# Kernel tuning notes

Measured on AMD Instinct MI355X. Metric: run time of the kernel, lower is better.

The kernel has to match this reference:

```python
import jax, jax.numpy as jnp
import numpy as np

N_NODES = 100000
N_EDGES = 1600000
IN_DIM, HID_DIM, OUT_DIM = 32, 64, 8


def sage_conv(x, src, dst, W_l, b_l, W_r, n_nodes):
    # PyG SAGEConv (aggr='mean', root_weight=True):
    # out_i = W_l @ mean_{j in N(i)} x_j + b_l + W_r @ x_i
    msg_sum = jax.ops.segment_sum(x[src], dst, num_segments=n_nodes)  # [N, F]
    deg = jax.ops.segment_sum(jnp.ones((src.shape[0],), x.dtype), dst,
                              num_segments=n_nodes)  # [N]
    agg = msg_sum / jnp.maximum(deg, 1.0)[:, None]
    return agg @ W_l.T + b_l + x @ W_r.T


def setup_inputs() -> dict:
    key = jax.random.key(0)
    ks = jax.random.split(key, 8)
    x = jax.random.normal(ks[0], (N_NODES, IN_DIM), dtype=jnp.float32)
    edge_index = jax.random.randint(ks[1], (2, N_EDGES), 0, N_NODES, dtype=jnp.int64)
    s1 = 1.0 / np.sqrt(IN_DIM)
    s2 = 1.0 / np.sqrt(HID_DIM)
    return {
        "x": x,
        "edge_index": edge_index,
        "W1_l": jax.random.uniform(ks[2], (HID_DIM, IN_DIM), jnp.float32, -s1, s1),
        "b1": jnp.zeros((HID_DIM,), jnp.float32),
        "W1_r": jax.random.uniform(ks[3], (HID_DIM, IN_DIM), jnp.float32, -s1, s1),
        "W2_l": jax.random.uniform(ks[4], (OUT_DIM, HID_DIM), jnp.float32, -s2, s2),
        "b2": jnp.zeros((OUT_DIM,), jnp.float32),
        "W2_r": jax.random.uniform(ks[5], (OUT_DIM, HID_DIM), jnp.float32, -s2, s2),
    }


def reference(x, edge_index, W1_l, b1, W1_r, W2_l, b2, W2_r):
    src, dst = edge_index[0], edge_index[1]
    h = sage_conv(x, src, dst, W1_l, b1, W1_r, N_NODES)
    h = jax.nn.relu(h)
    out = sage_conv(h, src, dst, W2_l, b2, W2_r, N_NODES)
    return out
```

## Files before the change

kernel.cpp:

```cpp
#include <hip/hip_runtime.h>

#define N_NODES 100000
#define N_EDGES 1600000
#define IN_DIM 32
#define HID_DIM 64
#define OUT_DIM 8
#define BK 64
#define NBKT ((N_NODES + BK - 1) / BK)
#define QC 1280
#define CHUNK 4096
#define NCHUNK ((N_EDGES + CHUNK - 1) / CHUNK)

typedef unsigned short u16;
typedef unsigned int u32;
typedef unsigned long long ull;

__device__ __forceinline__ float bf2f(u16 v) {
    return __uint_as_float(((u32)v) << 16);
}

__device__ __forceinline__ u16 f2bf(float f) {
    u32 u = __float_as_uint(f);
    u32 lsb = (u >> 16) & 1u;
    u += 0x7fffu + lsb;
    return (u16)(u >> 16);
}

__device__ __forceinline__ float ldf(const void* p, size_t i, int bf) {
    return bf ? bf2f(((const u16*)p)[i]) : ((const float*)p)[i];
}

__global__ __launch_bounds__(256) void k_part2(
    const int* __restrict__ ei, const u32* __restrict__ xw,
    const void* __restrict__ W1l, const void* __restrict__ b1,
    const void* __restrict__ W1r,
    const void* __restrict__ W2l, const void* __restrict__ b2,
    const void* __restrict__ W2r,
    int* __restrict__ qcnt, u32* __restrict__ qbuf,
    float* __restrict__ tW1l, float* __restrict__ tW1r,
    float* __restrict__ tW2l, float* __restrict__ tW2r,
    float* __restrict__ tb1, float* __restrict__ tb2)
{
    __shared__ int shv, bfv;
    __shared__ int hist[NBKT], gbase[NBKT], lcur[NBKT];
    int t = threadIdx.x;
    if (t < 64) {
        int v = ei[2 * t + 1];
        ull m1 = __ballot(v == 0);
        u32 wd = xw[t];
        u32 b = (wd >> 8) & 0x7fu;
        ull m2 = __ballot(b >= 0x38u && b <= 0x41u);
        if (t == 0) {
            shv = (m1 == ~0ULL) ? 1 : 0;
            bfv = (__popcll(m2) >= 56) ? 1 : 0;
        }
    }
    for (int i = t; i < NBKT; i += 256) { hist[i] = 0; lcur[i] = 0; }
    __syncthreads();
    int sh = shv, bf = bfv;

    if (blockIdx.x < 16) {
        for (int i = blockIdx.x * 256 + t; i < HID_DIM * IN_DIM; i += 16 * 256) {
            int o = i / IN_DIM, k = i % IN_DIM;
            tW1l[k * HID_DIM + o] = ldf(W1l, i, bf);
            tW1r[k * HID_DIM + o] = ldf(W1r, i, bf);
        }
        for (int i = blockIdx.x * 256 + t; i < OUT_DIM * HID_DIM; i += 16 * 256) {
            int o = i / HID_DIM, k = i % HID_DIM;
            tW2l[k * OUT_DIM + o] = ldf(W2l, i, bf);
            tW2r[k * OUT_DIM + o] = ldf(W2r, i, bf);
        }
        if (blockIdx.x == 0) {
            if (t < HID_DIM) tb1[t] = ldf(b1, t, bf);
            if (t < OUT_DIM) tb2[t] = ldf(b2, t, bf);
        }
    }

    int e0 = blockIdx.x * CHUNK;
    int myd[16], mys[16];
    #pragma unroll
    for (int i = 0; i < 16; i++) {
        int e = e0 + i * 256 + t;
        if (e < N_EDGES) {
            size_t off = (size_t)e << sh;
            mys[i] = ei[off];
            int d = ei[((size_t)N_EDGES << sh) + off];
            myd[i] = d;
            atomicAdd(&hist[d >> 6], 1);
        } else myd[i] = -1;
    }
    __syncthreads();
    for (int i = t; i < NBKT; i += 256) {
        int h = hist[i];
        gbase[i] = h ? atomicAdd(&qcnt[i], h) : 0;
    }
    __syncthreads();
    #pragma unroll
    for (int i = 0; i < 16; i++) {
        int d = myd[i];
        if (d >= 0) {
            int bk = d >> 6;
            int p = gbase[bk] + atomicAdd(&lcur[bk], 1);
            if (p < QC)
                qbuf[(size_t)bk * QC + p] = ((u32)mys[i] << 6) | (u32)(d & 63);
        }
    }
}

__global__ __launch_bounds__(256, 4) void k_l1(
    const void* __restrict__ x,
    const int* __restrict__ qcnt, const u32* __restrict__ qbuf,
    const float* __restrict__ tW1l, const float* __restrict__ tW1r,
    const float* __restrict__ tW2l, const float* __restrict__ tW2r,
    const float* __restrict__ tb1, const float* __restrict__ tb2,
    u16* __restrict__ gbuf, float* __restrict__ rbuf,
    const u32* __restrict__ xw)
{
    __shared__ int hist[BK], pos[BK], pcur[BK];
    __shared__ u32 srt[QC];
    __shared__ float xs[BK][IN_DIM];
    __shared__ float aggw[4][2][IN_DIM];
    __shared__ float hb[8][HID_DIM + 1];
    __shared__ int bfv;

    int t = threadIdx.x;
    if (t < 64) {
        u32 wd = xw[t];
        u32 b = (wd >> 8) & 0x7fu;
        ull m2 = __ballot(b >= 0x38u && b <= 0x41u);
        if (t == 0) bfv = (__popcll(m2) >= 56) ? 1 : 0;
    }
    if (t < BK) hist[t] = 0;
    __syncthreads();
    int bf = bfv;
    int b = blockIdx.x, nb = b * BK;
    int m = qcnt[b]; if (m > QC) m = QC; if (m < 0) m = 0;
    const u32* q = qbuf + (size_t)b * QC;

    if (bf) {
        const u32* xr = (const u32*)x + (size_t)nb * (IN_DIM / 2);
        int lim = ((N_NODES - nb < BK) ? (N_NODES - nb) : BK) * (IN_DIM / 2);
        for (int i = t; i < BK * (IN_DIM / 2); i += 256) {
            u32 w = (i < lim) ? xr[i] : 0u;
            int r = i >> 4, c = i & 15;
            xs[r][2 * c]     = bf2f((u16)w);
            xs[r][2 * c + 1] = bf2f((u16)(w >> 16));
        }
    } else {
        const float* xr = (const float*)x + (size_t)nb * IN_DIM;
        int lim = ((N_NODES - nb < BK) ? (N_NODES - nb) : BK) * IN_DIM;
        for (int i = t; i < BK * IN_DIM; i += 256)
            xs[i >> 5][i & 31] = (i < lim) ? xr[i] : 0.0f;
    }

    for (int i = t; i < m; i += 256)
        atomicAdd(&hist[q[i] & 63], 1);
    __syncthreads();
    if (t < 64) {
        int v = hist[t];
        int inc = v;
        #pragma unroll
        for (int o = 1; o < 64; o <<= 1) {
            int y = __shfl_up(inc, o, 64);
            if (t >= o) inc += y;
        }
        int ex = inc - v;
        pos[t] = ex; pcur[t] = ex;
    }
    __syncthreads();
    for (int i = t; i < m; i += 256) {
        u32 u = q[i];
        int p = atomicAdd(&pcur[u & 63], 1);
        srt[p] = u >> 6;
    }
    __syncthreads();

    int wid = t >> 6, lane = t & 63;
    int half = lane >> 5, g2 = (lane >> 3) & 3, l = lane & 7;
    int o = lane;
    float bb = tb1[o];
    for (int pr = 0; pr < 8; pr++) {
        int s0 = pr * 8 + wid * 2;
        int ns = s0 + half;
        int st = pos[ns], deg = hist[ns];
        float a0 = 0, a1 = 0, a2 = 0, a3 = 0;
        float c0 = 0, c1 = 0, c2 = 0, c3 = 0;
        float d0 = 0, d1 = 0, d2 = 0, d3 = 0;
        float e0 = 0, e1 = 0, e2 = 0, e3 = 0;
        int j = g2;
        for (; j + 12 < deg; j += 16) {
            int sA = (int)srt[st + j];
            int sB = (int)srt[st + j + 4];
            int sC = (int)srt[st + j + 8];
            int sD = (int)srt[st + j + 12];
            if (bf) {
                ushort4 vA = reinterpret_cast<const ushort4*>((const u16*)x + (size_t)sA * IN_DIM)[l];
                ushort4 vB = reinterpret_cast<const ushort4*>((const u16*)x + (size_t)sB * IN_DIM)[l];
                ushort4 vC = reinterpret_cast<const ushort4*>((const u16*)x + (size_t)sC * IN_DIM)[l];
                ushort4 vD = reinterpret_cast<const ushort4*>((const u16*)x + (size_t)sD * IN_DIM)[l];
                a0 += bf2f(vA.x); a1 += bf2f(vA.y); a2 += bf2f(vA.z); a3 += bf2f(vA.w);
                c0 += bf2f(vB.x); c1 += bf2f(vB.y); c2 += bf2f(vB.z); c3 += bf2f(vB.w);
                d0 += bf2f(vC.x); d1 += bf2f(vC.y); d2 += bf2f(vC.z); d3 += bf2f(vC.w);
                e0 += bf2f(vD.x); e1 += bf2f(vD.y); e2 += bf2f(vD.z); e3 += bf2f(vD.w);
            } else {
                float4 vA = reinterpret_cast<const float4*>((const float*)x + (size_t)sA * IN_DIM)[l];
                float4 vB = reinterpret_cast<const float4*>((const float*)x + (size_t)sB * IN_DIM)[l];
                float4 vC = reinterpret_cast<const float4*>((const float*)x + (size_t)sC * IN_DIM)[l];
                float4 vD = reinterpret_cast<const float4*>((const float*)x + (size_t)sD * IN_DIM)[l];
                a0 += vA.x; a1 += vA.y; a2 += vA.z; a3 += vA.w;
                c0 += vB.x; c1 += vB.y; c2 += vB.z; c3 += vB.w;
                d0 += vC.x; d1 += vC.y; d2 += vC.z; d3 += vC.w;
                e0 += vD.x; e1 += vD.y; e2 += vD.z; e3 += vD.w;
            }
        }
        for (; j + 4 < deg; j += 8) {
            int sA = (int)srt[st + j];
            int sB = (int)srt[st + j + 4];
            if (bf) {
                ushort4 vA = reinterpret_cast<const ushort4*>((const u16*)x + (size_t)sA * IN_DIM)[l];
                ushort4 vB = reinterpret_cast<const ushort4*>((const u16*)x + (size_t)sB * IN_DIM)[l];
                a0 += bf2f(vA.x); a1 += bf2f(vA.y); a2 += bf2f(vA.z); a3 += bf2f(vA.w);
                c0 += bf2f(vB.x); c1 += bf2f(vB.y); c2 += bf2f(vB.z); c3 += bf2f(vB.w);
            } else {
                float4 vA = reinterpret_cast<const float4*>((const float*)x + (size_t)sA * IN_DIM)[l];
                float4 vB = reinterpret_cast<const float4*>((const float*)x + (size_t)sB * IN_DIM)[l];
                a0 += vA.x; a1 += vA.y; a2 += vA.z; a3 += vA.w;
                c0 += vB.x; c1 += vB.y; c2 += vB.z; c3 += vB.w;
            }
        }
        if (j < deg) {
            int s = (int)srt[st + j];
            if (bf) {
                ushort4 vv = reinterpret_cast<const ushort4*>((const u16*)x + (size_t)s * IN_DIM)[l];
                a0 += bf2f(vv.x); a1 += bf2f(vv.y); a2 += bf2f(vv.z); a3 += bf2f(vv.w);
            } else {
                float4 vv = reinterpret_cast<const float4*>((const float*)x + (size_t)s * IN_DIM)[l];
                a0 += vv.x; a1 += vv.y; a2 += vv.z; a3 += vv.w;
            }
        }
        a0 += c0 + d0 + e0;
        a1 += c1 + d1 + e1;
        a2 += c2 + d2 + e2;
        a3 += c3 + d3 + e3;
        a0 += __shfl_xor(a0, 8, 64);  a0 += __shfl_xor(a0, 16, 64);
        a1 += __shfl_xor(a1, 8, 64);  a1 += __shfl_xor(a1, 16, 64);
        a2 += __shfl_xor(a2, 8, 64);  a2 += __shfl_xor(a2, 16, 64);
        a3 += __shfl_xor(a3, 8, 64);  a3 += __shfl_xor(a3, 16, 64);
        if (g2 == 0) {
            aggw[wid][half][4 * l + 0] = a0; aggw[wid][half][4 * l + 1] = a1;
            aggw[wid][half][4 * l + 2] = a2; aggw[wid][half][4 * l + 3] = a3;
        }
        float rd0 = 1.0f / fmaxf((float)hist[s0], 1.0f);
        float rd1 = 1.0f / fmaxf((float)hist[s0 + 1], 1.0f);
        float acc0 = bb, acc1 = bb;
        #pragma unroll 8
        for (int k = 0; k < IN_DIM; k++) {
            float wl = tW1l[k * HID_DIM + o];
            float wr = tW1r[k * HID_DIM + o];
            acc0 += (aggw[wid][0][k] * rd0) * wl + xs[s0][k] * wr;
            acc1 += (aggw[wid][1][k] * rd1) * wl + xs[s0 + 1][k] * wr;
        }
        hb[wid * 2][o]     = fmaxf(acc0, 0.0f);
        hb[wid * 2 + 1][o] = fmaxf(acc1, 0.0f);
        int hs = wid * 2 + half;
        float ga = 0.0f, ra = 0.0f;
        #pragma unroll 4
        for (int mm = 0; mm < 16; mm++) {
            int k = g2 * 16 + mm;
            float hv = hb[hs][k];
            ga += hv * tW2l[k * OUT_DIM + l];
            ra += hv * tW2r[k * OUT_DIM + l];
        }
        ga += __shfl_xor(ga, 8, 64);  ga += __shfl_xor(ga, 16, 64);
        ra += __shfl_xor(ra, 8, 64);  ra += __shfl_xor(ra, 16, 64);
        int n = nb + ns;
        if (g2 == 0 && n < N_NODES) {
            __builtin_nontemporal_store(f2bf(ga), &gbuf[(size_t)n * OUT_DIM + l]);
            __builtin_nontemporal_store(ra + tb2[l], &rbuf[(size_t)n * OUT_DIM + l]);
        }
    }
}

__global__ __launch_bounds__(256) void k_l2(
    const u16* __restrict__ gbuf, const float* __restrict__ rbuf,
    const int* __restrict__ qcnt, const u32* __restrict__ qbuf,
    const u32* __restrict__ xw, void* __restrict__ out)
{
    __shared__ int hist[BK], pos[BK], pcur[BK];
    __shared__ u32 srt[QC];
    __shared__ int bfv;
    int t = threadIdx.x;
    if (t < 64) {
        u32 w = xw[t];
        u32 b = (w >> 8) & 0x7fu;
        ull m2 = __ballot(b >= 0x38u && b <= 0x41u);
        if (t == 0) bfv = (__popcll(m2) >= 56) ? 1 : 0;
    }
    if (t < BK) hist[t] = 0;
    __syncthreads();
    int b = blockIdx.x, nb = b * BK;
    int m = qcnt[b]; if (m > QC) m = QC; if (m < 0) m = 0;
    const u32* q = qbuf + (size_t)b * QC;

    for (int i = t; i < m; i += 256)
        atomicAdd(&hist[q[i] & 63], 1);
    __syncthreads();
    if (t < 64) {
        int v = hist[t];
        int inc = v;
        #pragma unroll
        for (int o = 1; o < 64; o <<= 1) {
            int y = __shfl_up(inc, o, 64);
            if (t >= o) inc += y;
        }
        int ex = inc - v;
        pos[t] = ex; pcur[t] = ex;
    }
    __syncthreads();
    for (int i = t; i < m; i += 256) {
        u32 u = q[i];
        int p = atomicAdd(&pcur[u & 63], 1);
        srt[p] = u >> 6;
    }
    __syncthreads();

    int grp = t >> 3, l = t & 7;
    for (int r = 0; r < 2; r++) {
        int ns = grp * 2 + r;
        int st = pos[ns], deg = hist[ns];
        float a0 = 0.0f, a1 = 0.0f, a2 = 0.0f, a3 = 0.0f;
        int j = 0;
        for (; j + 3 < deg; j += 4) {
            int v0 = (int)srt[st + j];
            int v1 = (int)srt[st + j + 1];
            int v2 = (int)srt[st + j + 2];
            int v3 = (int)srt[st + j + 3];
            a0 += bf2f(gbuf[(size_t)v0 * OUT_DIM + l]);
            a1 += bf2f(gbuf[(size_t)v1 * OUT_DIM + l]);
            a2 += bf2f(gbuf[(size_t)v2 * OUT_DIM + l]);
            a3 += bf2f(gbuf[(size_t)v3 * OUT_DIM + l]);
        }
        for (; j < deg; j++) a0 += bf2f(gbuf[(size_t)srt[st + j] * OUT_DIM + l]);
        int n = nb + ns;
        if (n < N_NODES) {
            float res = (a0 + a1 + a2 + a3) / fmaxf((float)deg, 1.0f)
                      + rbuf[(size_t)n * OUT_DIM + l];
            size_t oi = (size_t)n * OUT_DIM + l;
            if (bfv) ((u16*)out)[oi] = f2bf(res);
            else     ((float*)out)[oi] = res;
        }
    }
}

extern "C" void kernel_launch(void* const* d_in, const int* in_sizes, int n_in,
                              void* d_out, int out_size, void* d_ws, size_t ws_size,
                              hipStream_t stream) {
    const void* x   = d_in[0];
    const int*  ei  = (const int*)d_in[1];
    const void* W1l = d_in[2];
    const void* b1  = d_in[3];
    const void* W1r = d_in[4];
    const void* W2l = d_in[5];
    const void* b2  = d_in[6];
    const void* W2r = d_in[7];

    int* qcnt    = (int*)d_ws;
    float* tW1l  = (float*)(qcnt + 2048);
    float* tW1r  = tW1l + IN_DIM * HID_DIM;
    float* tW2l  = tW1r + IN_DIM * HID_DIM;
    float* tW2r  = tW2l + HID_DIM * OUT_DIM;
    float* tb1   = tW2r + HID_DIM * OUT_DIM;
    float* tb2   = tb1 + HID_DIM;
    u32* qbuf    = (u32*)(tb2 + OUT_DIM);
    u16* gbuf    = (u16*)(qbuf + (size_t)NBKT * QC);
    float* rbuf  = (float*)(gbuf + (size_t)N_NODES * OUT_DIM);

    hipMemsetAsync(d_ws, 0, 2048 * sizeof(int), stream);

    k_part2<<<NCHUNK, 256, 0, stream>>>(ei, (const u32*)x,
                                        W1l, b1, W1r, W2l, b2, W2r,
                                        qcnt, qbuf,
                                        tW1l, tW1r, tW2l, tW2r, tb1, tb2);
    k_l1<<<NBKT, 256, 0, stream>>>(x, qcnt, qbuf,
                                   tW1l, tW1r, tW2l, tW2r, tb1, tb2,
                                   gbuf, rbuf, (const u32*)x);
    k_l2<<<NBKT, 256, 0, stream>>>(gbuf, rbuf, qcnt, qbuf,
                                   (const u32*)x, d_out);
}
```

Before: 213.9 us.

## Split x features into two half-width arrays and gather in two passes

The partition kernel now also copies x into two separate arrays holding the low and high 16 features of each node. The layer-1 gather runs in two passes, one per half, with 8 neighbor groups of 4 lanes each. Results go into a full-block shared agg buffer that the matmul stage reads. The aim is to shrink the gathered working set per pass so it stays in cache and improves locality. In exchange it adds an extra copy of x, more workspace, larger shared memory, and twice the index traversal. Several reads also switch to nontemporal loads.

```diff
diff --git a/kernel.cpp b/kernel.cpp
--- a/kernel.cpp
+++ b/kernel.cpp
@@ -39,7 +39,8 @@
     int* __restrict__ qcnt, u32* __restrict__ qbuf,
     float* __restrict__ tW1l, float* __restrict__ tW1r,
     float* __restrict__ tW2l, float* __restrict__ tW2r,
-    float* __restrict__ tb1, float* __restrict__ tb2)
+    float* __restrict__ tb1, float* __restrict__ tb2,
+    u32* __restrict__ xlo, u32* __restrict__ xhi)
 {
     __shared__ int shv, bfv;
     __shared__ int hist[NBKT], gbase[NBKT], lcur[NBKT];
@@ -59,6 +60,20 @@
     __syncthreads();
     int sh = shv, bf = bfv;
 
+    if (bf) {
+        for (int i = blockIdx.x * 256 + t; i < N_NODES * 8; i += NCHUNK * 256) {
+            int n2 = i >> 3, k = i & 7;
+            __builtin_nontemporal_store(xw[n2 * 16 + k], &xlo[i]);
+            __builtin_nontemporal_store(xw[n2 * 16 + 8 + k], &xhi[i]);
+        }
+    } else {
+        for (int i = blockIdx.x * 256 + t; i < N_NODES * 16; i += NCHUNK * 256) {
+            int n2 = i >> 4, k = i & 15;
+            __builtin_nontemporal_store(xw[n2 * 32 + k], &xlo[i]);
+            __builtin_nontemporal_store(xw[n2 * 32 + 16 + k], &xhi[i]);
+        }
+    }
+
     if (blockIdx.x < 16) {
         for (int i = blockIdx.x * 256 + t; i < HID_DIM * IN_DIM; i += 16 * 256) {
             int o = i / IN_DIM, k = i % IN_DIM;
@@ -108,6 +123,7 @@
 }
 
 __global__ __launch_bounds__(256, 4) void k_l1(
+    const void* __restrict__ xlo, const void* __restrict__ xhi,
     const void* __restrict__ x,
     const int* __restrict__ qcnt, const u32* __restrict__ qbuf,
     const float* __restrict__ tW1l, const float* __restrict__ tW1r,
@@ -119,7 +135,7 @@
     __shared__ int hist[BK], pos[BK], pcur[BK];
     __shared__ u32 srt[QC];
     __shared__ float xs[BK][IN_DIM];
-    __shared__ float aggw[4][2][IN_DIM];
+    __shared__ float agg[BK][IN_DIM];
     __shared__ float hb[8][HID_DIM + 1];
     __shared__ int bfv;
 
@@ -141,7 +157,7 @@
         const u32* xr = (const u32*)x + (size_t)nb * (IN_DIM / 2);
         int lim = ((N_NODES - nb < BK) ? (N_NODES - nb) : BK) * (IN_DIM / 2);
         for (int i = t; i < BK * (IN_DIM / 2); i += 256) {
-            u32 w = (i < lim) ? xr[i] : 0u;
+            u32 w = (i < lim) ? __builtin_nontemporal_load(&xr[i]) : 0u;
             int r = i >> 4, c = i & 15;
             xs[r][2 * c]     = bf2f((u16)w);
             xs[r][2 * c + 1] = bf2f((u16)(w >> 16));
@@ -150,11 +166,11 @@
         const float* xr = (const float*)x + (size_t)nb * IN_DIM;
         int lim = ((N_NODES - nb < BK) ? (N_NODES - nb) : BK) * IN_DIM;
         for (int i = t; i < BK * IN_DIM; i += 256)
-            xs[i >> 5][i & 31] = (i < lim) ? xr[i] : 0.0f;
+            xs[i >> 5][i & 31] = (i < lim) ? __builtin_nontemporal_load(&xr[i]) : 0.0f;
     }
 
     for (int i = t; i < m; i += 256)
-        atomicAdd(&hist[q[i] & 63], 1);
+        atomicAdd(&hist[__builtin_nontemporal_load(&q[i]) & 63], 1);
     __syncthreads();
     if (t < 64) {
         int v = hist[t];
@@ -169,87 +185,94 @@
     }
     __syncthreads();
     for (int i = t; i < m; i += 256) {
-        u32 u = q[i];
+        u32 u = __builtin_nontemporal_load(&q[i]);
         int p = atomicAdd(&pcur[u & 63], 1);
         srt[p] = u >> 6;
     }
     __syncthreads();
 
     int wid = t >> 6, lane = t & 63;
-    int half = lane >> 5, g2 = (lane >> 3) & 3, l = lane & 7;
+    int half = lane >> 5;
+    int g3 = (lane >> 2) & 7;
+    int l2 = lane & 3;
+    #pragma unroll
+    for (int pass = 0; pass < 2; pass++) {
+        const void* xh = pass ? xhi : xlo;
+        int kb = pass * 16 + l2 * 4;
+        for (int pr = 0; pr < 8; pr++) {
+            int ns = pr * 8 + wid * 2 + half;
+            int st = pos[ns], deg = hist[ns];
+            float a0 = 0, a1 = 0, a2 = 0, a3 = 0;
+            float c0 = 0, c1 = 0, c2 = 0, c3 = 0;
+            int j = g3;
+            for (; j + 24 < deg; j += 32) {
+                int sA = (int)srt[st + j];
+                int sB = (int)srt[st + j + 8];
+                int sC = (int)srt[st + j + 16];
+                int sD = (int)srt[st + j + 24];
+                if (bf) {
+                    ushort4 vA = reinterpret_cast<const ushort4*>((const u16*)xh + (size_t)sA * 16)[l2];
+                    ushort4 vB = reinterpret_cast<const ushort4*>((const u16*)xh + (size_t)sB * 16)[l2];
+                    ushort4 vC = reinterpret_cast<const ushort4*>((const u16*)xh + (size_t)sC * 16)[l2];
+                    ushort4 vD = reinterpret_cast<const ushort4*>((const u16*)xh + (size_t)sD * 16)[l2];
+                    a0 += bf2f(vA.x); a1 += bf2f(vA.y); a2 += bf2f(vA.z); a3 += bf2f(vA.w);
+                    c0 += bf2f(vB.x); c1 += bf2f(vB.y); c2 += bf2f(vB.z); c3 += bf2f(vB.w);
+                    a0 += bf2f(vC.x); a1 += bf2f(vC.y); a2 += bf2f(vC.z); a3 += bf2f(vC.w);
+                    c0 += bf2f(vD.x); c1 += bf2f(vD.y); c2 += bf2f(vD.z); c3 += bf2f(vD.w);
+                } else {
+                    float4 vA = reinterpret_cast<const float4*>((const float*)xh + (size_t)sA * 16)[l2];
+                    float4 vB = reinterpret_cast<const float4*>((const float*)xh + (size_t)sB * 16)[l2];
+                    float4 vC = reinterpret_cast<const float4*>((const float*)xh + (size_t)sC * 16)[l2];
+                    float4 vD = reinterpret_cast<const float4*>((const float*)xh + (size_t)sD * 16)[l2];
+                    a0 += vA.x; a1 += vA.y; a2 += vA.z; a3 += vA.w;
+                    c0 += vB.x; c1 += vB.y; c2 += vB.z; c3 += vB.w;
+                    a0 += vC.x; a1 += vC.y; a2 += vC.z; a3 += vC.w;
+                    c0 += vD.x; c1 += vD.y; c2 += vD.z; c3 += vD.w;
+                }
+            }
+            for (; j + 8 < deg; j += 16) {
+                int sA = (int)srt[st + j];
+                int sB = (int)srt[st + j + 8];
+                if (bf) {
+                    ushort4 vA = reinterpret_cast<const ushort4*>((const u16*)xh + (size_t)sA * 16)[l2];
+                    ushort4 vB = reinterpret_cast<const ushort4*>((const u16*)xh + (size_t)sB * 16)[l2];
+                    a0 += bf2f(vA.x); a1 += bf2f(vA.y); a2 += bf2f(vA.z); a3 += bf2f(vA.w);
+                    c0 += bf2f(vB.x); c1 += bf2f(vB.y); c2 += bf2f(vB.z); c3 += bf2f(vB.w);
+                } else {
+                    float4 vA = reinterpret_cast<const float4*>((const float*)xh + (size_t)sA * 16)[l2];
+                    float4 vB = reinterpret_cast<const float4*>((const float*)xh + (size_t)sB * 16)[l2];
+                    a0 += vA.x; a1 += vA.y; a2 += vA.z; a3 += vA.w;
+                    c0 += vB.x; c1 += vB.y; c2 += vB.z; c3 += vB.w;
+                }
+            }
+            if (j < deg) {
+                int s = (int)srt[st + j];
+                if (bf) {
+                    ushort4 vv = reinterpret_cast<const ushort4*>((const u16*)xh + (size_t)s * 16)[l2];
+                    a0 += bf2f(vv.x); a1 += bf2f(vv.y); a2 += bf2f(vv.z); a3 += bf2f(vv.w);
+                } else {
+                    float4 vv = reinterpret_cast<const float4*>((const float*)xh + (size_t)s * 16)[l2];
+                    a0 += vv.x; a1 += vv.y; a2 += vv.z; a3 += vv.w;
+                }
+            }
+            a0 += c0; a1 += c1; a2 += c2; a3 += c3;
+            a0 += __shfl_xor(a0, 4, 64); a0 += __shfl_xor(a0, 8, 64); a0 += __shfl_xor(a0, 16, 64);
+            a1 += __shfl_xor(a1, 4, 64); a1 += __shfl_xor(a1, 8, 64); a1 += __shfl_xor(a1, 16, 64);
+            a2 += __shfl_xor(a2, 4, 64); a2 += __shfl_xor(a2, 8, 64); a2 += __shfl_xor(a2, 16, 64);
+            a3 += __shfl_xor(a3, 4, 64); a3 += __shfl_xor(a3, 8, 64); a3 += __shfl_xor(a3, 16, 64);
+            if (g3 == 0) {
+                agg[ns][kb + 0] = a0; agg[ns][kb + 1] = a1;
+                agg[ns][kb + 2] = a2; agg[ns][kb + 3] = a3;
+            }
+        }
+    }
+
+    int g2 = (lane >> 3) & 3, l = lane & 7;
     int o = lane;
     float bb = tb1[o];
     for (int pr = 0; pr < 8; pr++) {
         int s0 = pr * 8 + wid * 2;
         int ns = s0 + half;
-        int st = pos[ns], deg = hist[ns];
-        float a0 = 0, a1 = 0, a2 = 0, a3 = 0;
-        float c0 = 0, c1 = 0, c2 = 0, c3 = 0;
-        float d0 = 0, d1 = 0, d2 = 0, d3 = 0;
-        float e0 = 0, e1 = 0, e2 = 0, e3 = 0;
-        int j = g2;
-        for (; j + 12 < deg; j += 16) {
-            int sA = (int)srt[st + j];
-            int sB = (int)srt[st + j + 4];
-            int sC = (int)srt[st + j + 8];
-            int sD = (int)srt[st + j + 12];
-            if (bf) {
-                ushort4 vA = reinterpret_cast<const ushort4*>((const u16*)x + (size_t)sA * IN_DIM)[l];
-                ushort4 vB = reinterpret_cast<const ushort4*>((const u16*)x + (size_t)sB * IN_DIM)[l];
-                ushort4 vC = reinterpret_cast<const ushort4*>((const u16*)x + (size_t)sC * IN_DIM)[l];
-                ushort4 vD = reinterpret_cast<const ushort4*>((const u16*)x + (size_t)sD * IN_DIM)[l];
-                a0 += bf2f(vA.x); a1 += bf2f(vA.y); a2 += bf2f(vA.z); a3 += bf2f(vA.w);
-                c0 += bf2f(vB.x); c1 += bf2f(vB.y); c2 += bf2f(vB.z); c3 += bf2f(vB.w);
-                d0 += bf2f(vC.x); d1 += bf2f(vC.y); d2 += bf2f(vC.z); d3 += bf2f(vC.w);
-                e0 += bf2f(vD.x); e1 += bf2f(vD.y); e2 += bf2f(vD.z); e3 += bf2f(vD.w);
-            } else {
-                float4 vA = reinterpret_cast<const float4*>((const float*)x + (size_t)sA * IN_DIM)[l];
-                float4 vB = reinterpret_cast<const float4*>((const float*)x + (size_t)sB * IN_DIM)[l];
-                float4 vC = reinterpret_cast<const float4*>((const float*)x + (size_t)sC * IN_DIM)[l];
-                float4 vD = reinterpret_cast<const float4*>((const float*)x + (size_t)sD * IN_DIM)[l];
-                a0 += vA.x; a1 += vA.y; a2 += vA.z; a3 += vA.w;
-                c0 += vB.x; c1 += vB.y; c2 += vB.z; c3 += vB.w;
-                d0 += vC.x; d1 += vC.y; d2 += vC.z; d3 += vC.w;
-                e0 += vD.x; e1 += vD.y; e2 += vD.z; e3 += vD.w;
-            }
-        }
-        for (; j + 4 < deg; j += 8) {
-            int sA = (int)srt[st + j];
-            int sB = (int)srt[st + j + 4];
-            if (bf) {
-                ushort4 vA = reinterpret_cast<const ushort4*>((const u16*)x + (size_t)sA * IN_DIM)[l];
-                ushort4 vB = reinterpret_cast<const ushort4*>((const u16*)x + (size_t)sB * IN_DIM)[l];
-                a0 += bf2f(vA.x); a1 += bf2f(vA.y); a2 += bf2f(vA.z); a3 += bf2f(vA.w);
-                c0 += bf2f(vB.x); c1 += bf2f(vB.y); c2 += bf2f(vB.z); c3 += bf2f(vB.w);
-            } else {
-                float4 vA = reinterpret_cast<const float4*>((const float*)x + (size_t)sA * IN_DIM)[l];
-                float4 vB = reinterpret_cast<const float4*>((const float*)x + (size_t)sB * IN_DIM)[l];
-                a0 += vA.x; a1 += vA.y; a2 += vA.z; a3 += vA.w;
-                c0 += vB.x; c1 += vB.y; c2 += vB.z; c3 += vB.w;
-            }
-        }
-        if (j < deg) {
-            int s = (int)srt[st + j];
-            if (bf) {
-                ushort4 vv = reinterpret_cast<const ushort4*>((const u16*)x + (size_t)s * IN_DIM)[l];
-                a0 += bf2f(vv.x); a1 += bf2f(vv.y); a2 += bf2f(vv.z); a3 += bf2f(vv.w);
-            } else {
-                float4 vv = reinterpret_cast<const float4*>((const float*)x + (size_t)s * IN_DIM)[l];
-                a0 += vv.x; a1 += vv.y; a2 += vv.z; a3 += vv.w;
-            }
-        }
-        a0 += c0 + d0 + e0;
-        a1 += c1 + d1 + e1;
-        a2 += c2 + d2 + e2;
-        a3 += c3 + d3 + e3;
-        a0 += __shfl_xor(a0, 8, 64);  a0 += __shfl_xor(a0, 16, 64);
-        a1 += __shfl_xor(a1, 8, 64);  a1 += __shfl_xor(a1, 16, 64);
-        a2 += __shfl_xor(a2, 8, 64);  a2 += __shfl_xor(a2, 16, 64);
-        a3 += __shfl_xor(a3, 8, 64);  a3 += __shfl_xor(a3, 16, 64);
-        if (g2 == 0) {
-            aggw[wid][half][4 * l + 0] = a0; aggw[wid][half][4 * l + 1] = a1;
-            aggw[wid][half][4 * l + 2] = a2; aggw[wid][half][4 * l + 3] = a3;
-        }
         float rd0 = 1.0f / fmaxf((float)hist[s0], 1.0f);
         float rd1 = 1.0f / fmaxf((float)hist[s0 + 1], 1.0f);
         float acc0 = bb, acc1 = bb;
@@ -257,8 +280,8 @@
         for (int k = 0; k < IN_DIM; k++) {
             float wl = tW1l[k * HID_DIM + o];
             float wr = tW1r[k * HID_DIM + o];
-            acc0 += (aggw[wid][0][k] * rd0) * wl + xs[s0][k] * wr;
-            acc1 += (aggw[wid][1][k] * rd1) * wl + xs[s0 + 1][k] * wr;
+            acc0 += (agg[s0][k] * rd0) * wl + xs[s0][k] * wr;
+            acc1 += (agg[s0 + 1][k] * rd1) * wl + xs[s0 + 1][k] * wr;
         }
         hb[wid * 2][o]     = fmaxf(acc0, 0.0f);
         hb[wid * 2 + 1][o] = fmaxf(acc1, 0.0f);
@@ -303,7 +326,7 @@
     const u32* q = qbuf + (size_t)b * QC;
 
     for (int i = t; i < m; i += 256)
-        atomicAdd(&hist[q[i] & 63], 1);
+        atomicAdd(&hist[__builtin_nontemporal_load(&q[i]) & 63], 1);
     __syncthreads();
     if (t < 64) {
         int v = hist[t];
@@ -318,7 +341,7 @@
     }
     __syncthreads();
     for (int i = t; i < m; i += 256) {
-        u32 u = q[i];
+        u32 u = __builtin_nontemporal_load(&q[i]);
         int p = atomicAdd(&pcur[u & 63], 1);
         srt[p] = u >> 6;
     }
@@ -374,14 +397,17 @@
     u32* qbuf    = (u32*)(tb2 + OUT_DIM);
     u16* gbuf    = (u16*)(qbuf + (size_t)NBKT * QC);
     float* rbuf  = (float*)(gbuf + (size_t)N_NODES * OUT_DIM);
+    u32* xlo     = (u32*)(rbuf + (size_t)N_NODES * OUT_DIM);
+    u32* xhi     = xlo + (size_t)N_NODES * 16;
 
     hipMemsetAsync(d_ws, 0, 2048 * sizeof(int), stream);
 
     k_part2<<<NCHUNK, 256, 0, stream>>>(ei, (const u32*)x,
                                         W1l, b1, W1r, W2l, b2, W2r,
                                         qcnt, qbuf,
-                                        tW1l, tW1r, tW2l, tW2r, tb1, tb2);
-    k_l1<<<NBKT, 256, 0, stream>>>(x, qcnt, qbuf,
+                                        tW1l, tW1r, tW2l, tW2r, tb1, tb2,
+                                        xlo, xhi);
+    k_l1<<<NBKT, 256, 0, stream>>>(xlo, xhi, x, qcnt, qbuf,
                                    tW1l, tW1r, tW2l, tW2r, tb1, tb2,
                                    gbuf, rbuf, (const u32*)x);
     k_l2<<<NBKT, 256, 0, stream>>>(gbuf, rbuf, qcnt, qbuf,
```

New measurement: 237.3 us. 11.0% more time.

## Split neighbor gather into two source-range passes for cache locality

Applied to the files above, without the earlier changes.

Edges for each destination block are binned by whether the source node falls in the lower or upper half of the node range, and the gather runs in two passes so that all blocks touch roughly the same half of x at a time. Aggregates go to a per-block shared agg array and are summed across passes before the dense layer. The aim is better L2/MALL hit rate on the random gathers. In exchange it adds a second scan, more shared memory (lower occupancy), and only global phase alignment between blocks, which is not guaranteed.

```diff
diff --git a/kernel.cpp b/kernel.cpp
--- a/kernel.cpp
+++ b/kernel.cpp
@@ -10,6 +10,7 @@
 #define QC 1280
 #define CHUNK 4096
 #define NCHUNK ((N_EDGES + CHUNK - 1) / CHUNK)
+#define SRC_MID 50000
 
 typedef unsigned short u16;
 typedef unsigned int u32;
@@ -116,12 +117,12 @@
     u16* __restrict__ gbuf, float* __restrict__ rbuf,
     const u32* __restrict__ xw)
 {
-    __shared__ int hist[BK], pos[BK], pcur[BK];
+    __shared__ int hist[2 * BK], pos[2 * BK], pcur[2 * BK];
     __shared__ u32 srt[QC];
     __shared__ float xs[BK][IN_DIM];
-    __shared__ float aggw[4][2][IN_DIM];
+    __shared__ float agg[BK][IN_DIM];
     __shared__ float hb[8][HID_DIM + 1];
-    __shared__ int bfv;
+    __shared__ int wtot, bfv;
 
     int t = threadIdx.x;
     if (t < 64) {
@@ -130,7 +131,7 @@
         ull m2 = __ballot(b >= 0x38u && b <= 0x41u);
         if (t == 0) bfv = (__popcll(m2) >= 56) ? 1 : 0;
     }
-    if (t < BK) hist[t] = 0;
+    if (t < 2 * BK) hist[t] = 0;
     __syncthreads();
     int bf = bfv;
     int b = blockIdx.x, nb = b * BK;
@@ -153,112 +154,129 @@
             xs[i >> 5][i & 31] = (i < lim) ? xr[i] : 0.0f;
     }
 
-    for (int i = t; i < m; i += 256)
-        atomicAdd(&hist[q[i] & 63], 1);
-    __syncthreads();
-    if (t < 64) {
-        int v = hist[t];
-        int inc = v;
+    for (int i = t; i < m; i += 256) {
+        u32 u = q[i];
+        int bin = (((int)(u >> 6) >= SRC_MID) ? BK : 0) | (int)(u & 63);
+        atomicAdd(&hist[bin], 1);
+    }
+    __syncthreads();
+    int inc = 0, v = 0;
+    if (t < 128) {
+        v = hist[t]; inc = v;
         #pragma unroll
         for (int o = 1; o < 64; o <<= 1) {
             int y = __shfl_up(inc, o, 64);
-            if (t >= o) inc += y;
-        }
-        int ex = inc - v;
+            if ((t & 63) >= o) inc += y;
+        }
+        if (t == 63) wtot = inc;
+    }
+    __syncthreads();
+    if (t < 128) {
+        int ex = ((t >= 64) ? wtot : 0) + inc - v;
         pos[t] = ex; pcur[t] = ex;
     }
     __syncthreads();
     for (int i = t; i < m; i += 256) {
         u32 u = q[i];
-        int p = atomicAdd(&pcur[u & 63], 1);
-        srt[p] = u >> 6;
+        int s = (int)(u >> 6);
+        int bin = ((s >= SRC_MID) ? BK : 0) | (int)(u & 63);
+        int p = atomicAdd(&pcur[bin], 1);
+        srt[p] = (u32)s;
     }
     __syncthreads();
 
     int wid = t >> 6, lane = t & 63;
     int half = lane >> 5, g2 = (lane >> 3) & 3, l = lane & 7;
+    for (int pass = 0; pass < 2; pass++) {
+        for (int pr = 0; pr < 8; pr++) {
+            int ns = pr * 8 + wid * 2 + half;
+            int bin = pass * BK + ns;
+            int st = pos[bin], dg = hist[bin];
+            float a0 = 0, a1 = 0, a2 = 0, a3 = 0;
+            float c0 = 0, c1 = 0, c2 = 0, c3 = 0;
+            float d0 = 0, d1 = 0, d2 = 0, d3 = 0;
+            float e0 = 0, e1 = 0, e2 = 0, e3 = 0;
+            int j = g2;
+            for (; j + 12 < dg; j += 16) {
+                int sA = (int)srt[st + j];
+                int sB = (int)srt[st + j + 4];
+                int sC = (int)srt[st + j + 8];
+                int sD = (int)srt[st + j + 12];
+                if (bf) {
+                    ushort4 vA = reinterpret_cast<const ushort4*>((const u16*)x + (size_t)sA * IN_DIM)[l];
+                    ushort4 vB = reinterpret_cast<const ushort4*>((const u16*)x + (size_t)sB * IN_DIM)[l];
+                    ushort4 vC = reinterpret_cast<const ushort4*>((const u16*)x + (size_t)sC * IN_DIM)[l];
+                    ushort4 vD = reinterpret_cast<const ushort4*>((const u16*)x + (size_t)sD * IN_DIM)[l];
+                    a0 += bf2f(vA.x); a1 += bf2f(vA.y); a2 += bf2f(vA.z); a3 += bf2f(vA.w);
+                    c0 += bf2f(vB.x); c1 += bf2f(vB.y); c2 += bf2f(vB.z); c3 += bf2f(vB.w);
+                    d0 += bf2f(vC.x); d1 += bf2f(vC.y); d2 += bf2f(vC.z); d3 += bf2f(vC.w);
+                    e0 += bf2f(vD.x); e1 += bf2f(vD.y); e2 += bf2f(vD.z); e3 += bf2f(vD.w);
+                } else {
+                    float4 vA = reinterpret_cast<const float4*>((const float*)x + (size_t)sA * IN_DIM)[l];
+                    float4 vB = reinterpret_cast<const float4*>((const float*)x + (size_t)sB * IN_DIM)[l];
+                    float4 vC = reinterpret_cast<const float4*>((const float*)x + (size_t)sC * IN_DIM)[l];
+                    float4 vD = reinterpret_cast<const float4*>((const float*)x + (size_t)sD * IN_DIM)[l];
+                    a0 += vA.x; a1 += vA.y; a2 += vA.z; a3 += vA.w;
+                    c0 += vB.x; c1 += vB.y; c2 += vB.z; c3 += vB.w;
+                    d0 += vC.x; d1 += vC.y; d2 += vC.z; d3 += vC.w;
+                    e0 += vD.x; e1 += vD.y; e2 += vD.z; e3 += vD.w;
+                }
+            }
+            for (; j + 4 < dg; j += 8) {
+                int sA = (int)srt[st + j];
+                int sB = (int)srt[st + j + 4];
+                if (bf) {
+                    ushort4 vA = reinterpret_cast<const ushort4*>((const u16*)x + (size_t)sA * IN_DIM)[l];
+                    ushort4 vB = reinterpret_cast<const ushort4*>((const u16*)x + (size_t)sB * IN_DIM)[l];
+                    a0 += bf2f(vA.x); a1 += bf2f(vA.y); a2 += bf2f(vA.z); a3 += bf2f(vA.w);
+                    c0 += bf2f(vB.x); c1 += bf2f(vB.y); c2 += bf2f(vB.z); c3 += bf2f(vB.w);
+                } else {
+                    float4 vA = reinterpret_cast<const float4*>((const float*)x + (size_t)sA * IN_DIM)[l];
+                    float4 vB = reinterpret_cast<const float4*>((const float*)x + (size_t)sB * IN_DIM)[l];
+                    a0 += vA.x; a1 += vA.y; a2 += vA.z; a3 += vA.w;
+                    c0 += vB.x; c1 += vB.y; c2 += vB.z; c3 += vB.w;
+                }
+            }
+            if (j < dg) {
+                int s = (int)srt[st + j];
+                if (bf) {
+                    ushort4 vv = reinterpret_cast<const ushort4*>((const u16*)x + (size_t)s * IN_DIM)[l];
+                    a0 += bf2f(vv.x); a1 += bf2f(vv.y); a2 += bf2f(vv.z); a3 += bf2f(vv.w);
+                } else {
+                    float4 vv = reinterpret_cast<const float4*>((const float*)x + (size_t)s * IN_DIM)[l];
+                    a0 += vv.x; a1 += vv.y; a2 += vv.z; a3 += vv.w;
+                }
+            }
+            a0 += c0 + d0 + e0;
+            a1 += c1 + d1 + e1;
+            a2 += c2 + d2 + e2;
+            a3 += c3 + d3 + e3;
+            a0 += __shfl_xor(a0, 8, 64);  a0 += __shfl_xor(a0, 16, 64);
+            a1 += __shfl_xor(a1, 8, 64);  a1 += __shfl_xor(a1, 16, 64);
+            a2 += __shfl_xor(a2, 8, 64);  a2 += __shfl_xor(a2, 16, 64);
+            a3 += __shfl_xor(a3, 8, 64);  a3 += __shfl_xor(a3, 16, 64);
+            if (g2 == 0) {
+                float* ar = &agg[ns][4 * l];
+                if (pass == 0) { ar[0] = a0; ar[1] = a1; ar[2] = a2; ar[3] = a3; }
+                else           { ar[0] += a0; ar[1] += a1; ar[2] += a2; ar[3] += a3; }
+            }
+        }
+    }
+
     int o = lane;
     float bb = tb1[o];
     for (int pr = 0; pr < 8; pr++) {
         int s0 = pr * 8 + wid * 2;
         int ns = s0 + half;
-        int st = pos[ns], deg = hist[ns];
-        float a0 = 0, a1 = 0, a2 = 0, a3 = 0;
-        float c0 = 0, c1 = 0, c2 = 0, c3 = 0;
-        float d0 = 0, d1 = 0, d2 = 0, d3 = 0;
-        float e0 = 0, e1 = 0, e2 = 0, e3 = 0;
-        int j = g2;
-        for (; j + 12 < deg; j += 16) {
-            int sA = (int)srt[st + j];
-            int sB = (int)srt[st + j + 4];
-            int sC = (int)srt[st + j + 8];
-            int sD = (int)srt[st + j + 12];
-            if (bf) {
-                ushort4 vA = reinterpret_cast<const ushort4*>((const u16*)x + (size_t)sA * IN_DIM)[l];
-                ushort4 vB = reinterpret_cast<const ushort4*>((const u16*)x + (size_t)sB * IN_DIM)[l];
-                ushort4 vC = reinterpret_cast<const ushort4*>((const u16*)x + (size_t)sC * IN_DIM)[l];
-                ushort4 vD = reinterpret_cast<const ushort4*>((const u16*)x + (size_t)sD * IN_DIM)[l];
-                a0 += bf2f(vA.x); a1 += bf2f(vA.y); a2 += bf2f(vA.z); a3 += bf2f(vA.w);
-                c0 += bf2f(vB.x); c1 += bf2f(vB.y); c2 += bf2f(vB.z); c3 += bf2f(vB.w);
-                d0 += bf2f(vC.x); d1 += bf2f(vC.y); d2 += bf2f(vC.z); d3 += bf2f(vC.w);
-                e0 += bf2f(vD.x); e1 += bf2f(vD.y); e2 += bf2f(vD.z); e3 += bf2f(vD.w);
-            } else {
-                float4 vA = reinterpret_cast<const float4*>((const float*)x + (size_t)sA * IN_DIM)[l];
-                float4 vB = reinterpret_cast<const float4*>((const float*)x + (size_t)sB * IN_DIM)[l];
-                float4 vC = reinterpret_cast<const float4*>((const float*)x + (size_t)sC * IN_DIM)[l];
-                float4 vD = reinterpret_cast<const float4*>((const float*)x + (size_t)sD * IN_DIM)[l];
-                a0 += vA.x; a1 += vA.y; a2 += vA.z; a3 += vA.w;
-                c0 += vB.x; c1 += vB.y; c2 += vB.z; c3 += vB.w;
-                d0 += vC.x; d1 += vC.y; d2 += vC.z; d3 += vC.w;
-                e0 += vD.x; e1 += vD.y; e2 += vD.z; e3 += vD.w;
-            }
-        }
-        for (; j + 4 < deg; j += 8) {
-            int sA = (int)srt[st + j];
-            int sB = (int)srt[st + j + 4];
-            if (bf) {
-                ushort4 vA = reinterpret_cast<const ushort4*>((const u16*)x + (size_t)sA * IN_DIM)[l];
-                ushort4 vB = reinterpret_cast<const ushort4*>((const u16*)x + (size_t)sB * IN_DIM)[l];
-                a0 += bf2f(vA.x); a1 += bf2f(vA.y); a2 += bf2f(vA.z); a3 += bf2f(vA.w);
-                c0 += bf2f(vB.x); c1 += bf2f(vB.y); c2 += bf2f(vB.z); c3 += bf2f(vB.w);
-            } else {
-                float4 vA = reinterpret_cast<const float4*>((const float*)x + (size_t)sA * IN_DIM)[l];
-                float4 vB = reinterpret_cast<const float4*>((const float*)x + (size_t)sB * IN_DIM)[l];
-                a0 += vA.x; a1 += vA.y; a2 += vA.z; a3 += vA.w;
-                c0 += vB.x; c1 += vB.y; c2 += vB.z; c3 += vB.w;
-            }
-        }
-        if (j < deg) {
-            int s = (int)srt[st + j];
-            if (bf) {
-                ushort4 vv = reinterpret_cast<const ushort4*>((const u16*)x + (size_t)s * IN_DIM)[l];
-                a0 += bf2f(vv.x); a1 += bf2f(vv.y); a2 += bf2f(vv.z); a3 += bf2f(vv.w);
-            } else {
-                float4 vv = reinterpret_cast<const float4*>((const float*)x + (size_t)s * IN_DIM)[l];
-                a0 += vv.x; a1 += vv.y; a2 += vv.z; a3 += vv.w;
-            }
-        }
-        a0 += c0 + d0 + e0;
-        a1 += c1 + d1 + e1;
-        a2 += c2 + d2 + e2;
-        a3 += c3 + d3 + e3;
-        a0 += __shfl_xor(a0, 8, 64);  a0 += __shfl_xor(a0, 16, 64);
-        a1 += __shfl_xor(a1, 8, 64);  a1 += __shfl_xor(a1, 16, 64);
-        a2 += __shfl_xor(a2, 8, 64);  a2 += __shfl_xor(a2, 16, 64);
-        a3 += __shfl_xor(a3, 8, 64);  a3 += __shfl_xor(a3, 16, 64);
-        if (g2 == 0) {
-            aggw[wid][half][4 * l + 0] = a0; aggw[wid][half][4 * l + 1] = a1;
-            aggw[wid][half][4 * l + 2] = a2; aggw[wid][half][4 * l + 3] = a3;
-        }
-        float rd0 = 1.0f / fmaxf((float)hist[s0], 1.0f);
-        float rd1 = 1.0f / fmaxf((float)hist[s0 + 1], 1.0f);
+        float rd0 = 1.0f / fmaxf((float)(hist[s0] + hist[BK + s0]), 1.0f);
+        float rd1 = 1.0f / fmaxf((float)(hist[s0 + 1] + hist[BK + s0 + 1]), 1.0f);
         float acc0 = bb, acc1 = bb;
         #pragma unroll 8
         for (int k = 0; k < IN_DIM; k++) {
             float wl = tW1l[k * HID_DIM + o];
             float wr = tW1r[k * HID_DIM + o];
-            acc0 += (aggw[wid][0][k] * rd0) * wl + xs[s0][k] * wr;
-            acc1 += (aggw[wid][1][k] * rd1) * wl + xs[s0 + 1][k] * wr;
+            acc0 += (agg[s0][k] * rd0) * wl + xs[s0][k] * wr;
+            acc1 += (agg[s0 + 1][k] * rd1) * wl + xs[s0 + 1][k] * wr;
         }
         hb[wid * 2][o]     = fmaxf(acc0, 0.0f);
         hb[wid * 2 + 1][o] = fmaxf(acc1, 0.0f);
```

Measured after the change: 222.9 us. 1.04x slower.

## Split bucket queues into eight partitions to reduce global atomic contention

Applied to the files above, without the earlier changes.

The edge-bucketing kernel now spreads its per-bucket global counters and queue slots across eight partitions chosen by block index, so fewer blocks contend on the same counter atomics. The consumer kernels read all eight partition counts, compute offsets, and gather the partitioned queues into a shared-memory staging array before sorting. Edge-index loads and queue reads also become nontemporal. This adds more shared memory per block and an extra gather step, and a partition holding more than 224 edges for one bucket would drop edges (average is 32 per partition).

```diff
diff --git a/kernel.cpp b/kernel.cpp
--- a/kernel.cpp
+++ b/kernel.cpp
@@ -8,6 +8,8 @@
 #define BK 64
 #define NBKT ((N_NODES + BK - 1) / BK)
 #define QC 1280
+#define QCP 224
+#define QSTR 2048
 #define CHUNK 4096
 #define NCHUNK ((N_EDGES + CHUNK - 1) / CHUNK)
 
@@ -44,6 +46,7 @@
     __shared__ int shv, bfv;
     __shared__ int hist[NBKT], gbase[NBKT], lcur[NBKT];
     int t = threadIdx.x;
+    int part = blockIdx.x & 7;
     if (t < 64) {
         int v = ei[2 * t + 1];
         ull m1 = __ballot(v == 0);
@@ -83,8 +86,8 @@
         int e = e0 + i * 256 + t;
         if (e < N_EDGES) {
             size_t off = (size_t)e << sh;
-            mys[i] = ei[off];
-            int d = ei[((size_t)N_EDGES << sh) + off];
+            mys[i] = __builtin_nontemporal_load(&ei[off]);
+            int d = __builtin_nontemporal_load(&ei[((size_t)N_EDGES << sh) + off]);
             myd[i] = d;
             atomicAdd(&hist[d >> 6], 1);
         } else myd[i] = -1;
@@ -92,7 +95,7 @@
     __syncthreads();
     for (int i = t; i < NBKT; i += 256) {
         int h = hist[i];
-        gbase[i] = h ? atomicAdd(&qcnt[i], h) : 0;
+        gbase[i] = h ? atomicAdd(&qcnt[part * QSTR + i], h) : 0;
     }
     __syncthreads();
     #pragma unroll
@@ -101,8 +104,9 @@
         if (d >= 0) {
             int bk = d >> 6;
             int p = gbase[bk] + atomicAdd(&lcur[bk], 1);
-            if (p < QC)
-                qbuf[(size_t)bk * QC + p] = ((u32)mys[i] << 6) | (u32)(d & 63);
+            if (p < QCP)
+                qbuf[((size_t)part * NBKT + bk) * QCP + p] =
+                    ((u32)mys[i] << 6) | (u32)(d & 63);
         }
     }
 }
@@ -117,6 +121,8 @@
     const u32* __restrict__ xw)
 {
     __shared__ int hist[BK], pos[BK], pcur[BK];
+    __shared__ int mp[8], mbase[8], mtv;
+    __shared__ u32 raw[QC];
     __shared__ u32 srt[QC];
     __shared__ float xs[BK][IN_DIM];
     __shared__ float aggw[4][2][IN_DIM];
@@ -131,11 +137,35 @@
         if (t == 0) bfv = (__popcll(m2) >= 56) ? 1 : 0;
     }
     if (t < BK) hist[t] = 0;
+    int b = blockIdx.x, nb = b * BK;
+    if (t < 8) {
+        int v = qcnt[t * QSTR + b];
+        if (v < 0) v = 0;
+        if (v > QCP) v = QCP;
+        mp[t] = v;
+    }
     __syncthreads();
     int bf = bfv;
-    int b = blockIdx.x, nb = b * BK;
-    int m = qcnt[b]; if (m > QC) m = QC; if (m < 0) m = 0;
-    const u32* q = qbuf + (size_t)b * QC;
+    if (t == 0) {
+        int s = 0;
+        for (int p = 0; p < 8; p++) {
+            mbase[p] = s;
+            int v = mp[p];
+            if (s + v > QC) v = QC - s;
+            if (v < 0) v = 0;
+            mp[p] = v; s += v;
+        }
+        mtv = s;
+    }
+    __syncthreads();
+    int m = mtv;
+
+    for (int p = 0; p < 8; p++) {
+        const u32* qp = qbuf + ((size_t)p * NBKT + b) * QCP;
+        int mpp = mp[p], mb = mbase[p];
+        for (int i = t; i < mpp; i += 256)
+            raw[mb + i] = __builtin_nontemporal_load(&qp[i]);
+    }
 
     if (bf) {
         const u32* xr = (const u32*)x + (size_t)nb * (IN_DIM / 2);
@@ -152,9 +182,10 @@
         for (int i = t; i < BK * IN_DIM; i += 256)
             xs[i >> 5][i & 31] = (i < lim) ? xr[i] : 0.0f;
     }
+    __syncthreads();
 
     for (int i = t; i < m; i += 256)
-        atomicAdd(&hist[q[i] & 63], 1);
+        atomicAdd(&hist[raw[i] & 63], 1);
     __syncthreads();
     if (t < 64) {
         int v = hist[t];
@@ -169,7 +200,7 @@
     }
     __syncthreads();
     for (int i = t; i < m; i += 256) {
-        u32 u = q[i];
+        u32 u = raw[i];
         int p = atomicAdd(&pcur[u & 63], 1);
         srt[p] = u >> 6;
     }
@@ -287,6 +318,8 @@
     const u32* __restrict__ xw, void* __restrict__ out)
 {
     __shared__ int hist[BK], pos[BK], pcur[BK];
+    __shared__ int mp[8], mbase[8], mtv;
+    __shared__ u32 raw[QC];
     __shared__ u32 srt[QC];
     __shared__ int bfv;
     int t = threadIdx.x;
@@ -297,13 +330,37 @@
         if (t == 0) bfv = (__popcll(m2) >= 56) ? 1 : 0;
     }
     if (t < BK) hist[t] = 0;
-    __syncthreads();
     int b = blockIdx.x, nb = b * BK;
-    int m = qcnt[b]; if (m > QC) m = QC; if (m < 0) m = 0;
-    const u32* q = qbuf + (size_t)b * QC;
+    if (t < 8) {
+        int v = qcnt[t * QSTR + b];
+        if (v < 0) v = 0;
+        if (v > QCP) v = QCP;
+        mp[t] = v;
+    }
+    __syncthreads();
+    if (t == 0) {
+        int s = 0;
+        for (int p = 0; p < 8; p++) {
+            mbase[p] = s;
+            int v = mp[p];
+            if (s + v > QC) v = QC - s;
+            if (v < 0) v = 0;
+            mp[p] = v; s += v;
+        }
+        mtv = s;
+    }
+    __syncthreads();
+    int m = mtv;
+    for (int p = 0; p < 8; p++) {
+        const u32* qp = qbuf + ((size_t)p * NBKT + b) * QCP;
+        int mpp = mp[p], mb = mbase[p];
+        for (int i = t; i < mpp; i += 256)
+            raw[mb + i] = __builtin_nontemporal_load(&qp[i]);
+    }
+    __syncthreads();
 
     for (int i = t; i < m; i += 256)
-        atomicAdd(&hist[q[i] & 63], 1);
+        atomicAdd(&hist[raw[i] & 63], 1);
     __syncthreads();
     if (t < 64) {
         int v = hist[t];
@@ -318,7 +375,7 @@
     }
     __syncthreads();
     for (int i = t; i < m; i += 256) {
-        u32 u = q[i];
+        u32 u = raw[i];
         int p = atomicAdd(&pcur[u & 63], 1);
         srt[p] = u >> 6;
     }
@@ -365,17 +422,17 @@
     const void* W2r = d_in[7];
 
     int* qcnt    = (int*)d_ws;
-    float* tW1l  = (float*)(qcnt + 2048);
+    float* tW1l  = (float*)(qcnt + 8 * QSTR);
     float* tW1r  = tW1l + IN_DIM * HID_DIM;
     float* tW2l  = tW1r + IN_DIM * HID_DIM;
     float* tW2r  = tW2l + HID_DIM * OUT_DIM;
     float* tb1   = tW2r + HID_DIM * OUT_DIM;
     float* tb2   = tb1 + HID_DIM;
     u32* qbuf    = (u32*)(tb2 + OUT_DIM);
-    u16* gbuf    = (u16*)(qbuf + (size_t)NBKT * QC);
+    u16* gbuf    = (u16*)(qbuf + (size_t)8 * NBKT * QCP);
     float* rbuf  = (float*)(gbuf + (size_t)N_NODES * OUT_DIM);
 
-    hipMemsetAsync(d_ws, 0, 2048 * sizeof(int), stream);
+    hipMemsetAsync(d_ws, 0, 8 * QSTR * sizeof(int), stream);
 
     k_part2<<<NCHUNK, 256, 0, stream>>>(ei, (const u32*)x,
                                         W1l, b1, W1r, W2l, b2, W2r,
```

Measured after the change: 213.5 us. About the same (-0.2%).
